# Performance work log

Measured on AMD Instinct MI355X. Metric: run time of the kernel, lower is better.

The kernel has to match this reference:

```python
import jax, jax.numpy as jnp
import numpy as np

B, A, D, E = 32, 1024, 384, 4   # batch, atoms, descriptor dim, n_elements
H1, H2 = 256, 192               # n_hidden = [256, 192]


def setup_inputs() -> dict:
    key = jax.random.key(0)
    ks = jax.random.split(key, 8)
    representation = jax.random.normal(ks[0], (B, A, D), dtype=jnp.float32)
    species = jax.random.randint(ks[1], (B, A), 0, E, dtype=jnp.int32)
    s = 0.05
    W1 = jax.random.normal(ks[2], (E, D, H1), dtype=jnp.float32) * s
    b1 = jax.random.normal(ks[3], (E, H1), dtype=jnp.float32) * s
    Wh = jax.random.normal(ks[4], (E, H1, H2), dtype=jnp.float32) * s
    bh = jax.random.normal(ks[5], (E, H2), dtype=jnp.float32) * s
    W2 = jax.random.normal(ks[6], (E, H2), dtype=jnp.float32) * s
    b2 = jax.random.normal(ks[7], (E,), dtype=jnp.float32) * s
    return {"representation": representation, "species": species,
            "W1": W1, "b1": b1, "Wh": Wh, "bh": bh, "W2": W2, "b2": b2}


def reference(representation, species, W1, b1, Wh, bh, W2, b2):
    # Dense compute of ALL element nets for every atom (faithful to torch code).
    # MLP: layer1 output is NOT activated (quirk of the original forward);
    # activation only applies to the intermediate `layers` list entries.
    h = jnp.einsum('bad,edh->baeh', representation, W1) + b1          # [B,A,E,H1]
    h = jax.nn.relu(jnp.einsum('baeh,ehk->baek', h, Wh) + bh)         # [B,A,E,H2]
    element_energies = jnp.einsum('baek,ek->bae', h, W2) + b2         # [B,A,E]
    onehot = jax.nn.one_hot(species, E, dtype=element_energies.dtype) # [B,A,E]
    energies = jnp.sum(onehot * element_energies, axis=(1, 2))        # [B]
    return energies
```

## Files before the change

### kernel.cpp

```cpp
#include <hip/hip_runtime.h>

typedef __attribute__((ext_vector_type(8))) short bf16x8;
typedef __attribute__((ext_vector_type(4))) float f32x4;
typedef unsigned short ushort_t;

#define NB 32
#define NA 1024
#define NATOMS (NB*NA)
#define D  384
#define H1 256
#define H2 192
#define NE 4
#define TA 64
#define NGRID 515

__device__ __forceinline__ ushort_t f2bf(float f) {
    union { float f; unsigned u; } v; v.f = f;
    unsigned r = v.u + 0x7FFF + ((v.u >> 16) & 1);
    return (ushort_t)(r >> 16);
}

__global__ __launch_bounds__(256) void scatter_kernel(
    const int* __restrict__ species, int* __restrict__ counts, int* __restrict__ bucket)
{
    __shared__ int wcnt[4][4];
    __shared__ int wbase[4][4];
    const int t = threadIdx.x, lane = t & 63, wv = t >> 6;
    const int i = blockIdx.x * 256 + t;
    const int e = species[i];

    unsigned long long m0 = __ballot(e == 0);
    unsigned long long m1 = __ballot(e == 1);
    unsigned long long m2 = __ballot(e == 2);
    unsigned long long m3 = __ballot(e == 3);
    unsigned long long mym = (e == 0) ? m0 : (e == 1) ? m1 : (e == 2) ? m2 : m3;
    const unsigned long long lt = (lane == 63) ? 0x7FFFFFFFFFFFFFFFull
                                               : ((1ull << lane) - 1ull);
    const int rank = __popcll(mym & lt);

    if (lane == 0) {
        wcnt[wv][0] = __popcll(m0); wcnt[wv][1] = __popcll(m1);
        wcnt[wv][2] = __popcll(m2); wcnt[wv][3] = __popcll(m3);
    }
    __syncthreads();
    if (t < NE) {
        int s = t;
        int tot = wcnt[0][s] + wcnt[1][s] + wcnt[2][s] + wcnt[3][s];
        int b = atomicAdd(&counts[s], tot);
        for (int w = 0; w < 4; ++w) { wbase[w][s] = b; b += wcnt[w][s]; }
    }
    __syncthreads();
    bucket[(e << 15) + wbase[wv][e] + rank] = i;
}

__global__ __launch_bounds__(256) void transpose_kernel(
    const float* __restrict__ W1, const float* __restrict__ Wh,
    ushort_t* __restrict__ w1t, ushort_t* __restrict__ wht,
    int* __restrict__ counts)
{
    if (blockIdx.x == 0 && threadIdx.x < NE) counts[threadIdx.x] = 0;
    __shared__ float tile[32][33];
    const int t = threadIdx.x;
    int bid = blockIdx.x;
    const float* src; ushort_t* dst; int R, C, e, rt, ct;
    if (bid < NE * 96) {
        e = bid / 96; int rem = bid % 96; rt = rem / 8; ct = rem % 8;
        src = W1; dst = w1t; R = D; C = H1;
    } else {
        bid -= NE * 96;
        e = bid / 48; int rem = bid % 48; rt = rem / 6; ct = rem % 6;
        src = Wh; dst = wht; R = H1; C = H2;
    }
    const float* S  = src + ((size_t)e * R + rt * 32) * C + ct * 32;
    ushort_t*    Dp = dst + ((size_t)e * C + ct * 32) * R + rt * 32;
    {
        int row = t >> 3, c4 = (t & 7) * 4;
        float4 v = *(const float4*)(S + (size_t)row * C + c4);
        tile[row][c4 + 0] = v.x; tile[row][c4 + 1] = v.y;
        tile[row][c4 + 2] = v.z; tile[row][c4 + 3] = v.w;
    }
    __syncthreads();
    {
        int orow = t >> 3, k4 = (t & 7) * 4;
        ushort4 o;
        o.x = f2bf(tile[k4 + 0][orow]);
        o.y = f2bf(tile[k4 + 1][orow]);
        o.z = f2bf(tile[k4 + 2][orow]);
        o.w = f2bf(tile[k4 + 3][orow]);
        *(ushort4*)(Dp + (size_t)orow * R + k4) = o;
    }
}

__global__ __launch_bounds__(512, 4) void mlp_kernel(
    const float*    __restrict__ rep,
    const int*      __restrict__ counts,
    const int*      __restrict__ bucket,
    const ushort_t* __restrict__ w1t,
    const ushort_t* __restrict__ wht,
    const float*    __restrict__ b1,
    const float*    __restrict__ bh,
    const float*    __restrict__ W2,
    const float*    __restrict__ b2,
    float*          __restrict__ energy)
{
    const int c0 = counts[0], c1 = counts[1], c2 = counts[2], c3 = counts[3];
    const int t0 = (c0 + 63) >> 6, t1 = (c1 + 63) >> 6, t2 = (c2 + 63) >> 6;
    const int t3 = (c3 + 63) >> 6;
    int bid = blockIdx.x;
    int e, tile, n;
    if      (bid < t0)                { e = 0; tile = bid;                n = c0; }
    else if (bid < t0 + t1)           { e = 1; tile = bid - t0;           n = c1; }
    else if (bid < t0 + t1 + t2)      { e = 2; tile = bid - t0 - t1;      n = c2; }
    else if (bid < t0 + t1 + t2 + t3) { e = 3; tile = bid - t0 - t1 - t2; n = c3; }
    else return;
    const int base = tile * TA;

    const int t    = threadIdx.x;
    const int lane = t & 63;
    const int wv   = t >> 6;
    const int g    = lane >> 4;
    const int r    = lane & 15;
    const int r7   = r & 7;

    __shared__ ushort_t smem[TA * D];
    ushort_t* Xt  = smem;
    ushort_t* H1t = smem;
    float*    eparts = (float*)(smem + 20480);

    {
        const int srow = t >> 3, scs = t & 7, sswz = srow & 7;
        int ai = base + srow;
        int gs = bucket[(e << 15) + (ai < n ? ai : base)];
        const float* xp = rep + (size_t)gs * D;
        #pragma unroll
        for (int i = 0; i < 6; ++i) {
            const int cs = scs + 8 * i;
            float4 v0 = *(const float4*)(xp + cs * 8);
            float4 v1 = *(const float4*)(xp + cs * 8 + 4);
            union { bf16x8 v; ushort_t u[8]; } pk;
            pk.u[0] = f2bf(v0.x); pk.u[1] = f2bf(v0.y);
            pk.u[2] = f2bf(v0.z); pk.u[3] = f2bf(v0.w);
            pk.u[4] = f2bf(v1.x); pk.u[5] = f2bf(v1.y);
            pk.u[6] = f2bf(v1.z); pk.u[7] = f2bf(v1.w);
            *(bf16x8*)(Xt + srow * D + ((cs ^ sswz) << 3)) = pk.v;
        }
    }
    __syncthreads();

    const ushort_t* a1p = w1t + ((size_t)e * H1 + wv * 32 + r) * D + g * 8;
    const int koff1 = (bid & 3) * 3;

    f32x4 acc1[2][4];
    #pragma unroll
    for (int nn = 0; nn < 2; ++nn)
        #pragma unroll
        for (int m = 0; m < 4; ++m)
            acc1[nn][m] = (f32x4){0.f, 0.f, 0.f, 0.f};

    uint4 afc[2], afn[2];
    {
        int k0 = koff1 * 32;
        afc[0] = *(const uint4*)(a1p + k0);
        afc[1] = *(const uint4*)(a1p + 16 * D + k0);
    }
    for (int ks = 0; ks < 12; ++ks) {
        int kse = ks + koff1; if (kse >= 12) kse -= 12;
        if (ks < 11) {
            int ksn = kse + 1; if (ksn >= 12) ksn -= 12;
            afn[0] = *(const uint4*)(a1p + ksn * 32);
            afn[1] = *(const uint4*)(a1p + 16 * D + ksn * 32);
        }
        bf16x8 bx[4];
        #pragma unroll
        for (int m = 0; m < 4; ++m) {
            const int cs = kse * 4 + g;
            bx[m] = *(const bf16x8*)(Xt + (m * 16 + r) * D + ((cs ^ r7) << 3));
        }
        #pragma unroll
        for (int nn = 0; nn < 2; ++nn)
            #pragma unroll
            for (int m = 0; m < 4; ++m)
                acc1[nn][m] = __builtin_amdgcn_mfma_f32_16x16x32_bf16(
                    __builtin_bit_cast(bf16x8, afc[nn]), bx[m], acc1[nn][m], 0, 0, 0);
        afc[0] = afn[0]; afc[1] = afn[1];
    }
    __syncthreads();

    #pragma unroll
    for (int nn = 0; nn < 2; ++nn) {
        float bv[4];
        #pragma unroll
        for (int q = 0; q < 4; ++q)
            bv[q] = b1[e * H1 + wv * 32 + nn * 16 + g * 4 + q];
        #pragma unroll
        for (int m = 0; m < 4; ++m) {
            unsigned p0 = f2bf(acc1[nn][m][0] + bv[0]);
            unsigned p1 = f2bf(acc1[nn][m][1] + bv[1]);
            unsigned p2 = f2bf(acc1[nn][m][2] + bv[2]);
            unsigned p3 = f2bf(acc1[nn][m][3] + bv[3]);
            uint2 pk; pk.x = p0 | (p1 << 16); pk.y = p2 | (p3 << 16);
            const int col = wv * 32 + nn * 16 + g * 4;
            const int cs  = col >> 3;
            const int phys = (m * 16 + r) * H1 + ((cs ^ r7) << 3) + (col & 7);
            *(uint2*)(H1t + phys) = pk;
        }
    }
    __syncthreads();

    f32x4 acc2[2][4];
    #pragma unroll
    for (int nn = 0; nn < 2; ++nn)
        #pragma unroll
        for (int m = 0; m < 4; ++m)
            acc2[nn][m] = (f32x4){0.f, 0.f, 0.f, 0.f};

    if (wv < 6) {
        const ushort_t* a2p = wht + ((size_t)e * H2 + wv * 32 + r) * H1 + g * 8;
        const int koff2 = (bid & 3) * 2;
        uint4 af2c[2], af2n[2];
        {
            int k0 = koff2 * 32;
            af2c[0] = *(const uint4*)(a2p + k0);
            af2c[1] = *(const uint4*)(a2p + 16 * H1 + k0);
        }
        for (int ks = 0; ks < 8; ++ks) {
            int kse = ks + koff2; if (kse >= 8) kse -= 8;
            if (ks < 7) {
                int ksn = kse + 1; if (ksn >= 8) ksn -= 8;
                af2n[0] = *(const uint4*)(a2p + ksn * 32);
                af2n[1] = *(const uint4*)(a2p + 16 * H1 + ksn * 32);
            }
            bf16x8 bx[4];
            #pragma unroll
            for (int m = 0; m < 4; ++m) {
                const int cs = kse * 4 + g;
                bx[m] = *(const bf16x8*)(H1t + (m * 16 + r) * H1 + ((cs ^ r7) << 3));
            }
            #pragma unroll
            for (int nn = 0; nn < 2; ++nn)
                #pragma unroll
                for (int m = 0; m < 4; ++m)
                    acc2[nn][m] = __builtin_amdgcn_mfma_f32_16x16x32_bf16(
                        __builtin_bit_cast(bf16x8, af2c[nn]), bx[m], acc2[nn][m], 0, 0, 0);
            af2c[0] = af2n[0]; af2c[1] = af2n[1];
        }

        #pragma unroll
        for (int m = 0; m < 4; ++m) {
            float s = 0.f;
            #pragma unroll
            for (int nn = 0; nn < 2; ++nn) {
                float bhv[4], w2v[4];
                #pragma unroll
                for (int q = 0; q < 4; ++q) {
                    int h2i = e * H2 + wv * 32 + nn * 16 + g * 4 + q;
                    bhv[q] = bh[h2i];
                    w2v[q] = W2[h2i];
                }
                #pragma unroll
                for (int q = 0; q < 4; ++q) {
                    float z = acc2[nn][m][q] + bhv[q];
                    z = fmaxf(z, 0.f);
                    s += z * w2v[q];
                }
            }
            s += __shfl_xor(s, 16, 64);
            s += __shfl_xor(s, 32, 64);
            if (lane < 16) eparts[wv * TA + m * 16 + r] = s;
        }
    }
    __syncthreads();

    if (t < TA) {
        int ai = base + t;
        if (ai < n) {
            int gi = bucket[(e << 15) + ai];
            float tot = b2[e];
            #pragma unroll
            for (int w = 0; w < 6; ++w) tot += eparts[w * TA + t];
            energy[gi] = tot;
        }
    }
}

__global__ void reduce_kernel(const float* __restrict__ energy, float* __restrict__ out) {
    const int b = blockIdx.x, t = threadIdx.x;
    float s = 0.f;
    for (int i = t; i < NA; i += 256) s += energy[b * NA + i];
    for (int off = 32; off > 0; off >>= 1) s += __shfl_down(s, off, 64);
    __shared__ float ws[4];
    if ((t & 63) == 0) ws[t >> 6] = s;
    __syncthreads();
    if (t == 0) out[b] = ws[0] + ws[1] + ws[2] + ws[3];
}

extern "C" void kernel_launch(void* const* d_in, const int* in_sizes, int n_in,
                              void* d_out, int out_size, void* d_ws, size_t ws_size,
                              hipStream_t stream) {
    const float* rep     = (const float*)d_in[0];
    const int*   species = (const int*)  d_in[1];
    const float* W1      = (const float*)d_in[2];
    const float* b1      = (const float*)d_in[3];
    const float* Wh      = (const float*)d_in[4];
    const float* bh      = (const float*)d_in[5];
    const float* W2      = (const float*)d_in[6];
    const float* b2      = (const float*)d_in[7];
    float* out = (float*)d_out;

    char* ws = (char*)d_ws;
    int*      counts  = (int*)      (ws + 0);
    int*      bucket  = (int*)      (ws + 64);
    float*    energy  = (float*)    (ws + 524352);
    ushort_t* w1t     = (ushort_t*) (ws + 655424);
    ushort_t* wht     = (ushort_t*) (ws + 1441856);

    transpose_kernel<<<NE * 96 + NE * 48, 256, 0, stream>>>(W1, Wh, w1t, wht, counts);
    scatter_kernel<<<NATOMS / 256, 256, 0, stream>>>(species, counts, bucket);
    mlp_kernel<<<NGRID, 512, 0, stream>>>(rep, counts, bucket, w1t, wht,
                                          b1, bh, W2, b2, energy);
    reduce_kernel<<<NB, 256, 0, stream>>>(energy, out);
}
```

Measured before the change: 127.0 us.

## Deepen weight-fragment prefetch to four stages and issue it before the staging barrier

Replaces the one-step-ahead register double buffer for the W1 and Wh MFMA operands with a four-deep ring buffer in fully unrolled loops. The first four W1 fragments are loaded before the activation tile is staged into shared memory, and the first Wh fragments are loaded before the layer-1 epilogue, so global latency overlaps the staging and bias work. This costs extra VGPRs, which may reduce occupancy or cause spills.

```diff
diff --git a/kernel.cpp b/kernel.cpp
--- a/kernel.cpp
+++ b/kernel.cpp
@@ -120,12 +120,25 @@
     const int wv   = t >> 6;
     const int g    = lane >> 4;
     const int r    = lane & 15;
-    const int r7   = r & 7;
+    const int r7   = r & 15 & 7;
 
     __shared__ ushort_t smem[TA * D];
     ushort_t* Xt  = smem;
     ushort_t* H1t = smem;
     float*    eparts = (float*)(smem + 20480);
+
+    const int koff1 = (bid & 3) * 3;
+    const int koff2 = (bid & 3) * 2;
+    const ushort_t* a1p = w1t + ((size_t)e * H1 + wv * 32 + r) * D + g * 8;
+    const ushort_t* a2p = wht + ((size_t)e * H2 + wv * 32 + r) * H1 + g * 8;
+
+    uint4 af[4][2];
+    #pragma unroll
+    for (int p = 0; p < 4; ++p) {
+        int kse = p + koff1; if (kse >= 12) kse -= 12;
+        af[p][0] = *(const uint4*)(a1p + kse * 32);
+        af[p][1] = *(const uint4*)(a1p + 16 * D + kse * 32);
+    }
 
     {
         const int srow = t >> 3, scs = t & 7, sswz = srow & 7;
@@ -147,9 +160,6 @@
     }
     __syncthreads();
 
-    const ushort_t* a1p = w1t + ((size_t)e * H1 + wv * 32 + r) * D + g * 8;
-    const int koff1 = (bid & 3) * 3;
-
     f32x4 acc1[2][4];
     #pragma unroll
     for (int nn = 0; nn < 2; ++nn)
@@ -157,19 +167,9 @@
         for (int m = 0; m < 4; ++m)
             acc1[nn][m] = (f32x4){0.f, 0.f, 0.f, 0.f};
 
-    uint4 afc[2], afn[2];
-    {
-        int k0 = koff1 * 32;
-        afc[0] = *(const uint4*)(a1p + k0);
-        afc[1] = *(const uint4*)(a1p + 16 * D + k0);
-    }
+    #pragma unroll
     for (int ks = 0; ks < 12; ++ks) {
         int kse = ks + koff1; if (kse >= 12) kse -= 12;
-        if (ks < 11) {
-            int ksn = kse + 1; if (ksn >= 12) ksn -= 12;
-            afn[0] = *(const uint4*)(a1p + ksn * 32);
-            afn[1] = *(const uint4*)(a1p + 16 * D + ksn * 32);
-        }
         bf16x8 bx[4];
         #pragma unroll
         for (int m = 0; m < 4; ++m) {
@@ -181,10 +181,24 @@
             #pragma unroll
             for (int m = 0; m < 4; ++m)
                 acc1[nn][m] = __builtin_amdgcn_mfma_f32_16x16x32_bf16(
-                    __builtin_bit_cast(bf16x8, afc[nn]), bx[m], acc1[nn][m], 0, 0, 0);
-        afc[0] = afn[0]; afc[1] = afn[1];
-    }
-    __syncthreads();
+                    __builtin_bit_cast(bf16x8, af[ks & 3][nn]), bx[m], acc1[nn][m], 0, 0, 0);
+        if (ks + 4 < 12) {
+            int ksn = ks + 4 + koff1; if (ksn >= 12) ksn -= 12;
+            af[ks & 3][0] = *(const uint4*)(a1p + ksn * 32);
+            af[ks & 3][1] = *(const uint4*)(a1p + 16 * D + ksn * 32);
+        }
+    }
+    __syncthreads();
+
+    uint4 af2[4][2];
+    if (wv < 6) {
+        #pragma unroll
+        for (int p = 0; p < 4; ++p) {
+            int kse = p + koff2; if (kse >= 8) kse -= 8;
+            af2[p][0] = *(const uint4*)(a2p + kse * 32);
+            af2[p][1] = *(const uint4*)(a2p + 16 * H1 + kse * 32);
+        }
+    }
 
     #pragma unroll
     for (int nn = 0; nn < 2; ++nn) {
@@ -215,21 +229,9 @@
             acc2[nn][m] = (f32x4){0.f, 0.f, 0.f, 0.f};
 
     if (wv < 6) {
-        const ushort_t* a2p = wht + ((size_t)e * H2 + wv * 32 + r) * H1 + g * 8;
-        const int koff2 = (bid & 3) * 2;
-        uint4 af2c[2], af2n[2];
-        {
-            int k0 = koff2 * 32;
-            af2c[0] = *(const uint4*)(a2p + k0);
-            af2c[1] = *(const uint4*)(a2p + 16 * H1 + k0);
-        }
+        #pragma unroll
         for (int ks = 0; ks < 8; ++ks) {
             int kse = ks + koff2; if (kse >= 8) kse -= 8;
-            if (ks < 7) {
-                int ksn = kse + 1; if (ksn >= 8) ksn -= 8;
-                af2n[0] = *(const uint4*)(a2p + ksn * 32);
-                af2n[1] = *(const uint4*)(a2p + 16 * H1 + ksn * 32);
-            }
             bf16x8 bx[4];
             #pragma unroll
             for (int m = 0; m < 4; ++m) {
@@ -241,8 +243,12 @@
                 #pragma unroll
                 for (int m = 0; m < 4; ++m)
                     acc2[nn][m] = __builtin_amdgcn_mfma_f32_16x16x32_bf16(
-                        __builtin_bit_cast(bf16x8, af2c[nn]), bx[m], acc2[nn][m], 0, 0, 0);
-            af2c[0] = af2n[0]; af2c[1] = af2n[1];
+                        __builtin_bit_cast(bf16x8, af2[ks & 3][nn]), bx[m], acc2[nn][m], 0, 0, 0);
+            if (ks + 4 < 8) {
+                int ksn = ks + 4 + koff2; if (ksn >= 8) ksn -= 8;
+                af2[ks & 3][0] = *(const uint4*)(a2p + ksn * 32);
+                af2[ks & 3][1] = *(const uint4*)(a2p + 16 * H1 + ksn * 32);
+            }
         }
 
         #pragma unroll
```

Result: no change. 126.8 us (-0.2%).
